# Kernel tuning notes

Measured on AMD Instinct MI355X. Metric: run time of the kernel, lower is better.

Reference implementation:

```python
import jax, jax.numpy as jnp
import numpy as np

B, T, C = 2, 2048, 1024
H, DH = 16, 64          # n_heads = d_model // 64
WIN = 256               # sliding window size
K = 32                  # n_oscillators
DFF = 4096              # d_ff_hidden
NEG = -1e9


def setup_inputs() -> dict:
    key = jax.random.key(0)
    ks = jax.random.split(key, 16)
    sC = 1.0 / np.sqrt(C)
    sF = 1.0 / np.sqrt(DFF)
    sK = 1.0 / np.sqrt(K)
    return {
        "x": jax.random.normal(ks[0], (B, T, C), jnp.float32),
        "norm1_w": jnp.ones((C,), jnp.float32),
        "qkv_w": jax.random.normal(ks[1], (3 * C, C), jnp.float32) * sC,
        "qkv_b": jnp.zeros((3 * C,), jnp.float32),
        "proj_w": jax.random.normal(ks[2], (C, C), jnp.float32) * sC,
        "proj_b": jnp.zeros((C,), jnp.float32),
        "gate_w": jax.random.normal(ks[3], (1, C), jnp.float32) * 0.01,
        "gate_b": jnp.zeros((1,), jnp.float32),
        "trn_win": jax.random.normal(ks[4], (K, C), jnp.float32) * sC,
        "trn_wout": jax.random.normal(ks[5], (C, K), jnp.float32) * sK,
        "trn_gate_w": jax.random.normal(ks[6], (K, C), jnp.float32) * sC,
        "trn_gate_b": jnp.zeros((K,), jnp.float32),
        "trn_a_logit": jax.random.normal(ks[7], (K,), jnp.float32),
        "trn_theta": jax.random.uniform(ks[8], (K,), jnp.float32, 0.0, np.pi),
        "trn_res_scale": jnp.asarray(0.1, jnp.float32),
        "norm2_w": jnp.ones((C,), jnp.float32),
        "ffn_gate_w": jax.random.normal(ks[9], (DFF, C), jnp.float32) * sC,
        "ffn_up_w": jax.random.normal(ks[10], (DFF, C), jnp.float32) * sC,
        "ffn_down_w": jax.random.normal(ks[11], (C, DFF), jnp.float32) * sF,
    }


def _rms(z, w, eps=1e-6):
    return z * jax.lax.rsqrt(jnp.mean(z * z, axis=-1, keepdims=True) + eps) * w


def reference(x, norm1_w, qkv_w, qkv_b, proj_w, proj_b, gate_w, gate_b,
              trn_win, trn_wout, trn_gate_w, trn_gate_b, trn_a_logit,
              trn_theta, trn_res_scale, norm2_w, ffn_gate_w, ffn_up_w,
              ffn_down_w):
    h = _rms(x, norm1_w)

    # ---- windowed causal attention (dense mask, as in the original) ----
    qkv = h @ qkv_w.T + qkv_b                       # [B,T,3C]
    q, k, v = jnp.split(qkv, 3, axis=-1)
    heads = lambda t: t.reshape(B, T, H, DH).transpose(0, 2, 1, 3)  # [B,H,T,DH]
    q, k, v = heads(q), heads(k), heads(v)
    row = jnp.arange(T)[:, None]
    col = jnp.arange(T)[None, :]
    mask = jnp.where((col <= row) & (col >= row - WIN + 1), 0.0, NEG).astype(x.dtype)
    scores = jnp.einsum('bhqd,bhkd->bhqk', q, k) / jnp.sqrt(jnp.asarray(DH, x.dtype))
    attn = jax.nn.softmax(scores + mask, axis=-1)
    ao = jnp.einsum('bhqk,bhkd->bhqd', attn, v).transpose(0, 2, 1, 3).reshape(B, T, C)
    ao = ao @ proj_w.T + proj_b

    # ---- temporal resonance branch: K damped rotating oscillators ----
    u = h @ trn_win.T                               # [B,T,K] drive
    a = jax.nn.sigmoid(trn_a_logit)                 # amplitude in (0,1) (amplitude_max=1)
    ct, st = jnp.cos(trn_theta), jnp.sin(trn_theta)

    def step(carry, ut):
        sr, si = carry
        nsr = a * (ct * sr - st * si) + ut
        nsi = a * (st * sr + ct * si)
        return (nsr, nsi), nsr

    init = (jnp.zeros((B, K), x.dtype), jnp.zeros((B, K), x.dtype))
    _, ys = jax.lax.scan(step, init, u.transpose(1, 0, 2))  # ys: [T,B,K]
    y = ys.transpose(1, 0, 2)                                # [B,T,K]
    tg = jax.nn.sigmoid(h @ trn_gate_w.T + trn_gate_b)
    trn_out = ((tg * y) @ trn_wout.T) * trn_res_scale        # [B,T,C]

    # ---- sigmoid gate mix + residual ----
    g = jax.nn.sigmoid(h @ gate_w.T + gate_b)       # [B,T,1]
    x = x + g * ao + (1.0 - g) * trn_out

    # ---- SwiGLU FFN ----
    h2 = _rms(x, norm2_w)
    ffn = (jax.nn.silu(h2 @ ffn_gate_w.T) * (h2 @ ffn_up_w.T)) @ ffn_down_w.T
    return x + ffn
```

## Files before the change

kernel.cpp:

```cpp
#include <hip/hip_runtime.h>


typedef unsigned short u16;
typedef unsigned short u16x8 __attribute__((ext_vector_type(8)));
typedef __bf16 bf16x8 __attribute__((ext_vector_type(8)));
typedef float f32x4 __attribute__((ext_vector_type(4)));

#define DI static __device__ __forceinline__

DI u16 f2b(float f){
  union { float f; unsigned u; } v; v.f = f;
  unsigned r = v.u + 0x7FFFu + ((v.u >> 16) & 1u);
  return (u16)(r >> 16);
}
DI float b2f(u16 b){
  union { unsigned u; float f; } v; v.u = ((unsigned)b) << 16; return v.f;
}
DI u16x8 ld8(const u16* p){ return *(const u16x8*)p; }

DI f32x4 MFMA16(u16x8 a, u16x8 b, f32x4 c){
  return __builtin_amdgcn_mfma_f32_16x16x32_bf16(
      __builtin_bit_cast(bf16x8, a), __builtin_bit_cast(bf16x8, b), c, 0, 0, 0);
}

DI void async16(const void* g, void* l){
  void* gg = const_cast<void*>(g);
  __builtin_amdgcn_global_load_lds(
      (__attribute__((address_space(1))) void*)gg,
      (__attribute__((address_space(3))) void*)l, 16, 0, 0);
}

__global__ __launch_bounds__(256) void prep_kernel(
    const float* __restrict__ qkvw, const float* __restrict__ projw,
    const float* __restrict__ fgw, const float* __restrict__ fuw,
    const float* __restrict__ fdw, const float* __restrict__ twin,
    const float* __restrict__ tgw, const float* __restrict__ twout,
    u16* __restrict__ dst,
    const float* __restrict__ x, const float* __restrict__ n1w,
    const float* __restrict__ gw, const float* __restrict__ gb,
    u16* __restrict__ h, float* __restrict__ g)
{
  const int blk = blockIdx.x, tid = threadIdx.x;
  if (blk < 16640){
    size_t i = (size_t)blk * 256 + tid;
    if (i >= 4259840u) return;
    size_t e = i * 4;
    float4 v;
    if (e < 3145728u)        v = *(const float4*)(qkvw + e);
    else if (e < 3276800u){
      size_t i2 = e - 3145728u;
      int row = (int)(i2 >> 10), c = (int)(i2 & 1023);
      if (row < 32)      v = *(const float4*)(twin + row * 1024 + c);
      else if (row < 64) v = *(const float4*)(tgw + (row - 32) * 1024 + c);
      else               v = make_float4(0.f, 0.f, 0.f, 0.f);
    }
    else if (e < 4456448u){
      unsigned i2 = (unsigned)(e - 3276800u);
      unsigned row = i2 / 1152u, kk = i2 - row * 1152u;
      if (kk < 1024u)      v = *(const float4*)(projw + (size_t)row * 1024 + kk);
      else if (kk < 1056u) v = *(const float4*)(twout + (size_t)row * 32 + (kk - 1024u));
      else                 v = make_float4(0.f, 0.f, 0.f, 0.f);
    }
    else if (e < 12845056u){
      size_t i2 = e - 4456448u;
      int row = (int)(i2 >> 10), c = (int)(i2 & 1023);
      int G = row >> 5, j = row & 31;
      const float* src = (j < 16) ? fgw : fuw;
      v = *(const float4*)(src + (size_t)(G * 16 + (j & 15)) * 1024 + c);
    }
    else                   v = *(const float4*)(fdw + (e - 12845056u));
    uint2 p;
    p.x = (unsigned)f2b(v.x) | ((unsigned)f2b(v.y) << 16);
    p.y = (unsigned)f2b(v.z) | ((unsigned)f2b(v.w) << 16);
    *(uint2*)(dst + e) = p;
    return;
  }
  const int row = blk - 16640;
  const int wave = tid >> 6, lane = tid & 63;
  __shared__ float sb[8];
  float4 xv = ((const float4*)(x + (size_t)row * 1024))[tid];
  float ss = xv.x*xv.x + xv.y*xv.y + xv.z*xv.z + xv.w*xv.w;
#pragma unroll
  for (int m = 32; m; m >>= 1) ss += __shfl_xor(ss, m);
  if (lane == 0) sb[wave] = ss;
  __syncthreads();
  float rstd = rsqrtf((sb[0]+sb[1]+sb[2]+sb[3]) * (1.f/1024.f) + 1e-6f);
  float4 wv = ((const float4*)n1w)[tid];
  float h0 = xv.x*rstd*wv.x, h1 = xv.y*rstd*wv.y;
  float h2v = xv.z*rstd*wv.z, h3 = xv.w*rstd*wv.w;
  uint2 pk;
  pk.x = (unsigned)f2b(h0) | ((unsigned)f2b(h1) << 16);
  pk.y = (unsigned)f2b(h2v) | ((unsigned)f2b(h3) << 16);
  ((uint2*)(h + (size_t)row * 1024))[tid] = pk;
  float4 gv = ((const float4*)gw)[tid];
  float gd = h0*gv.x + h1*gv.y + h2v*gv.z + h3*gv.w;
#pragma unroll
  for (int m = 32; m; m >>= 1) gd += __shfl_xor(gd, m);
  if (lane == 0) sb[4 + wave] = gd;
  __syncthreads();
  if (tid == 0) g[row] = 1.f / (1.f + __expf(-(sb[4]+sb[5]+sb[6]+sb[7] + gb[0])));
}

__global__ __launch_bounds__(256) void reduce_mix_norm(
    const u16* __restrict__ part, const float* __restrict__ x,
    const float* __restrict__ g, const float* __restrict__ pb,
    const float* __restrict__ n2w,
    float* __restrict__ out, u16* __restrict__ h2)
{
  const int row = blockIdx.x, tid = threadIdx.x;
  const int wave = tid >> 6, lane = tid & 63;
  __shared__ float sb[4];
  const size_t ro = (size_t)row * 1024;
  uint2 a0 = ((const uint2*)(part + ro))[tid];
  uint2 a1 = ((const uint2*)(part + 4194304 + ro))[tid];
  float4 bb = ((const float4*)pb)[tid];
  float4 xv = ((const float4*)(x + ro))[tid];
  float gg = g[row];
  float m0 = xv.x + b2f((u16)a0.x) + b2f((u16)a1.x) + gg*bb.x;
  float m1 = xv.y + b2f((u16)(a0.x >> 16)) + b2f((u16)(a1.x >> 16)) + gg*bb.y;
  float m2 = xv.z + b2f((u16)a0.y) + b2f((u16)a1.y) + gg*bb.z;
  float m3 = xv.w + b2f((u16)(a0.y >> 16)) + b2f((u16)(a1.y >> 16)) + gg*bb.w;
  float4 mo; mo.x = m0; mo.y = m1; mo.z = m2; mo.w = m3;
  ((float4*)(out + ro))[tid] = mo;
  float ss = m0*m0 + m1*m1 + m2*m2 + m3*m3;
#pragma unroll
  for (int m = 32; m; m >>= 1) ss += __shfl_xor(ss, m);
  if (lane == 0) sb[wave] = ss;
  __syncthreads();
  float rstd = rsqrtf((sb[0]+sb[1]+sb[2]+sb[3]) * (1.f/1024.f) + 1e-6f);
  float4 wv = ((const float4*)n2w)[tid];
  uint2 pk;
  pk.x = (unsigned)f2b(m0*rstd*wv.x) | ((unsigned)f2b(m1*rstd*wv.y) << 16);
  pk.y = (unsigned)f2b(m2*rstd*wv.z) | ((unsigned)f2b(m3*rstd*wv.w) << 16);
  ((uint2*)(h2 + ro))[tid] = pk;
}

__global__ __launch_bounds__(256) void reduce_down(
    const u16* __restrict__ part, float* __restrict__ out)
{
  size_t i = (size_t)blockIdx.x * 256 + threadIdx.x;
  uint2 a0 = ((const uint2*)part)[i];
  uint2 a1 = ((const uint2*)(part + 4194304))[i];
  uint2 a2 = ((const uint2*)(part + 8388608))[i];
  uint2 a3 = ((const uint2*)(part + 12582912))[i];
  float4 xv = ((float4*)out)[i];
  float4 o;
  o.x = xv.x + b2f((u16)a0.x) + b2f((u16)a1.x) + b2f((u16)a2.x) + b2f((u16)a3.x);
  o.y = xv.y + b2f((u16)(a0.x >> 16)) + b2f((u16)(a1.x >> 16))
             + b2f((u16)(a2.x >> 16)) + b2f((u16)(a3.x >> 16));
  o.z = xv.z + b2f((u16)a0.y) + b2f((u16)a1.y) + b2f((u16)a2.y) + b2f((u16)a3.y);
  o.w = xv.w + b2f((u16)(a0.y >> 16)) + b2f((u16)(a1.y >> 16))
             + b2f((u16)(a2.y >> 16)) + b2f((u16)(a3.y >> 16));
  ((float4*)out)[i] = o;
}

template<int MODE>
__global__ __launch_bounds__(256) void gemm_bt(
    const u16* __restrict__ A, const u16* __restrict__ B,
    float* __restrict__ outF, float* __restrict__ outF2, u16* __restrict__ outB,
    const float* __restrict__ bias, const float* __restrict__ auxF,
    int M, int N, int K)
{
  __shared__ __align__(16) u16 sA[2][128 * 32];
  __shared__ __align__(16) u16 sB[2][128 * 32];
  const int tid = threadIdx.x;
  const int wave = tid >> 6, lane = tid & 63;
  const int lr = lane & 15, lq = lane >> 4;
  const int m0 = blockIdx.x * 128, n0 = blockIdx.y * 128;
  const int wm = (wave & 1) * 64, wn = (wave >> 1) * 64;
  const int ks = K / (int)gridDim.z;
  const int kbeg = (int)blockIdx.z * ks, kend = kbeg + ks;
  f32x4 acc[4][4] = {};
  const int srow = wave * 16 + (lane >> 2);
  const int scol = (((lane & 3) ^ ((lane >> 3) & 3))) * 8;
  const u16* gA = A + (size_t)(m0 + srow) * K + scol;
  const u16* gB = B + (size_t)(n0 + srow) * K + scol;
  u16* lA0 = &sA[0][(wave * 16) * 32];
  u16* lA1 = &sA[0][(64 + wave * 16) * 32];
  u16* lB0 = &sB[0][(wave * 16) * 32];
  u16* lB1 = &sB[0][(64 + wave * 16) * 32];
  const size_t K64 = (size_t)64 * K;
  const int BUF = 128 * 32;
  const int ca = (lq ^ ((lr >> 1) & 3)) * 8;

  for (int k0 = kbeg; k0 < kend; k0 += 64){
    async16(gA + k0,            lA0);
    async16(gA + K64 + k0,      lA1);
    async16(gB + k0,            lB0);
    async16(gB + K64 + k0,      lB1);
    async16(gA + k0 + 32,       lA0 + BUF);
    async16(gA + K64 + k0 + 32, lA1 + BUF);
    async16(gB + k0 + 32,       lB0 + BUF);
    async16(gB + K64 + k0 + 32, lB1 + BUF);
    __syncthreads();
#pragma unroll
    for (int buf = 0; buf < 2; buf++){
      u16x8 af[4], bf[4];
#pragma unroll
      for (int i = 0; i < 4; i++) af[i] = ld8(&sA[buf][(wm + i*16 + lr)*32 + ca]);
#pragma unroll
      for (int i = 0; i < 4; i++) bf[i] = ld8(&sB[buf][(wn + i*16 + lr)*32 + ca]);
#pragma unroll
      for (int mi = 0; mi < 4; mi++)
#pragma unroll
        for (int ni = 0; ni < 4; ni++)
          acc[mi][ni] = MFMA16(af[mi], bf[ni], acc[mi][ni]);
    }
    __syncthreads();
  }

  if (MODE == 7){
    const int cb = ((n0 + wn) >> 1) + lr;
#pragma unroll
    for (int mi = 0; mi < 4; mi++){
      const int row = m0 + wm + mi*16 + lq*4;
#pragma unroll
      for (int p = 0; p < 2; p++){
        const int col = cb + p*16;
#pragma unroll
        for (int r = 0; r < 4; r++){
          float gv = acc[mi][2*p][r], uv = acc[mi][2*p+1][r];
          float rv = gv / (1.f + __expf(-gv)) * uv;
          outB[(size_t)(row + r) * (N >> 1) + col] = f2b(rv);
        }
      }
    }
    return;
  }

#pragma unroll
  for (int mi = 0; mi < 4; mi++){
    const int row = m0 + wm + mi*16 + lq*4;
#pragma unroll
    for (int ni = 0; ni < 4; ni++){
      const int col = n0 + wn + ni*16 + lr;
#pragma unroll
      for (int r = 0; r < 4; r++){
        const int rr = row + r;
        float v = acc[mi][ni][r];
        if (MODE == 0){
          if (n0 < 3072){
            outB[(size_t)rr * 3072 + col] = f2b(v + bias[col]);
          } else {
            int c2 = col - 3072;
            int bb = rr >> 11, tt = rr & 2047;
            if (c2 < 32) outF[((size_t)bb * 32 + c2) * 2048 + tt] = v;
            else if (c2 < 64)
              outF2[(size_t)rr * 32 + (c2 - 32)] =
                  1.f / (1.f + __expf(-(v + auxF[c2 - 32])));
          }
        } else if (MODE == 9){
          outB[(size_t)blockIdx.z * (size_t)M + (size_t)rr * N + col] = f2b(v);
        }
      }
    }
  }
}

__global__ __launch_bounds__(256) void attn_scan(
    const u16* __restrict__ qkv, const float* __restrict__ g,
    const float* __restrict__ u_t, const float* __restrict__ tg,
    const float* __restrict__ alog, const float* __restrict__ theta,
    const float* __restrict__ tscale, u16* __restrict__ Ap)
{
  __shared__ __align__(16) u16 sVt[64 * 72];
  __shared__ __align__(16) u16 sP[4][16 * 72];
  __shared__ float4 sc[256];
  const int blk = blockIdx.x, tid = threadIdx.x;

  if (blk < 1024){
    const int tile = blk & 31, hh = (blk >> 5) & 15, b = blk >> 9;
    const int t0 = tile * 64;
    const int wave = tid >> 6, lane = tid & 63;
    const int lr = lane & 15, lq = lane >> 4;
    const int qt = t0 + wave * 16;

    const u16* base = qkv + (size_t)b * 2048 * 3072 + hh * 64;
    const u16* qrow = base + (size_t)(qt + lr) * 3072 + lq * 8;
    u16x8 qf0 = ld8(qrow), qf1 = ld8(qrow + 32);
    const u16* kbase = base + 1024;
    const u16* vbase = base + 2048;

    f32x4 o0 = {0,0,0,0}, o1 = {0,0,0,0}, o2 = {0,0,0,0}, o3 = {0,0,0,0};
    float lsum[4] = {0.f, 0.f, 0.f, 0.f};
    const float c1 = 0.125f * 1.44269504088896f;

    const int kb = (t0 >= 256) ? (t0 - 256) : 0;
    const int ntl = (t0 + 64 - kb) >> 6;
    for (int it = 0; it < ntl; ++it){
      const int kt = kb + it * 64;
      __syncthreads();
      {
        const int key = tid & 63, dseg = tid >> 6;
        const u16* gv = vbase + (size_t)(kt + key) * 3072 + dseg * 16;
        u16x8 v0 = ld8(gv), v1 = ld8(gv + 8);
#pragma unroll
        for (int j = 0; j < 8; j++){
          sVt[(dseg*16 + j)     * 72 + key] = v0[j];
          sVt[(dseg*16 + 8 + j) * 72 + key] = v1[j];
        }
      }
      __syncthreads();
      const bool active = (kt < qt + 16) && (kt + 318 >= qt);
      if (!active) continue;

      f32x4 s[4] = {};
#pragma unroll
      for (int gK = 0; gK < 4; gK++){
        const u16* kr = kbase + (size_t)(kt + gK*16 + lr) * 3072 + lq * 8;
        u16x8 k0 = ld8(kr), k1 = ld8(kr + 32);
        s[gK] = MFMA16(qf0, k0, s[gK]);
        s[gK] = MFMA16(qf1, k1, s[gK]);
      }
#pragma unroll
      for (int r = 0; r < 4; r++){
        const int q = qt + lq * 4 + r;
#pragma unroll
        for (int gK = 0; gK < 4; gK++){
          const int c = kt + gK*16 + lr;
          float p = (c <= q && c + 255 >= q) ? exp2f(s[gK][r] * c1) : 0.f;
          lsum[r] += p;
          sP[wave][(lq*4 + r) * 72 + gK*16 + lr] = f2b(p);
        }
      }
      __builtin_amdgcn_s_waitcnt(0xc07f);
      u16x8 pf0 = ld8(&sP[wave][lr * 72 + lq * 8]);
      u16x8 pf1 = ld8(&sP[wave][lr * 72 + 32 + lq * 8]);
      o0 = MFMA16(pf0, ld8(&sVt[(lr)      * 72 + lq * 8]), o0);
      o0 = MFMA16(pf1, ld8(&sVt[(lr)      * 72 + 32 + lq * 8]), o0);
      o1 = MFMA16(pf0, ld8(&sVt[(16 + lr) * 72 + lq * 8]), o1);
      o1 = MFMA16(pf1, ld8(&sVt[(16 + lr) * 72 + 32 + lq * 8]), o1);
      o2 = MFMA16(pf0, ld8(&sVt[(32 + lr) * 72 + lq * 8]), o2);
      o2 = MFMA16(pf1, ld8(&sVt[(32 + lr) * 72 + 32 + lq * 8]), o2);
      o3 = MFMA16(pf0, ld8(&sVt[(48 + lr) * 72 + lq * 8]), o3);
      o3 = MFMA16(pf1, ld8(&sVt[(48 + lr) * 72 + 32 + lq * 8]), o3);
    }

#pragma unroll
    for (int r = 0; r < 4; r++){
      float l = lsum[r];
      l += __shfl_xor(l, 1); l += __shfl_xor(l, 2);
      l += __shfl_xor(l, 4); l += __shfl_xor(l, 8);
      lsum[r] = l;
    }

    const int trow = b * 2048 + qt + lq * 4;
    u16* aor = Ap + (size_t)trow * 1152 + hh * 64 + lr;
#pragma unroll
    for (int r = 0; r < 4; r++){
      float inv = g[trow + r] / lsum[r];
      u16* p = aor + (size_t)r * 1152;
      p[0]  = f2b(o0[r] * inv);
      p[16] = f2b(o1[r] * inv);
      p[32] = f2b(o2[r] * inv);
      p[48] = f2b(o3[r] * inv);
    }
    return;
  }

  if (blk < 1088){
    const int bk = blk - 1024;
    const int b = bk >> 5, k = bk & 31;
    const int j = tid;
    const float a = 1.f / (1.f + __expf(-alog[k]));
    const float th = theta[k];
    const float rs = tscale[0];
    const float wr = a * __cosf(th), wi = a * __sinf(th);
    const float* ubp = u_t + ((size_t)b * 32 + k) * 2048 + j * 8;
    float4 ua = ((const float4*)ubp)[0];
    float4 ub4 = ((const float4*)ubp)[1];
    float ur[8] = {ua.x, ua.y, ua.z, ua.w, ub4.x, ub4.y, ub4.z, ub4.w};
    float sr = 0.f, si = 0.f;
#pragma unroll
    for (int i = 0; i < 8; i++){
      float nr = wr*sr - wi*si + ur[i];
      float ni = wi*sr + wr*si;
      sr = nr; si = ni;
    }
    float w2r = wr*wr - wi*wi, w2i = 2.f*wr*wi;
    float w4r = w2r*w2r - w2i*w2i, w4i = 2.f*w2r*w2i;
    float Ar = w4r*w4r - w4i*w4i, Ai = 2.f*w4r*w4i;
    float4 cur; cur.x = Ar; cur.y = Ai; cur.z = sr; cur.w = si;
    sc[j] = cur;
    __syncthreads();
    for (int s = 1; s < 256; s <<= 1){
      float4 pv;
      const bool has = (j >= s);
      if (has) pv = sc[j - s];
      __syncthreads();
      if (has){
        float nar = cur.x*pv.x - cur.y*pv.y;
        float nai = cur.x*pv.y + cur.y*pv.x;
        float nbr = cur.x*pv.z - cur.y*pv.w + cur.z;
        float nbi = cur.x*pv.w + cur.y*pv.z + cur.w;
        cur.x = nar; cur.y = nai; cur.z = nbr; cur.w = nbi;
      }
      sc[j] = cur;
      __syncthreads();
    }
    float s_r = 0.f, s_i = 0.f;
    if (j > 0){ float4 pr = sc[j - 1]; s_r = pr.z; s_i = pr.w; }
    const int bt0 = b * 2048 + j * 8;
    const float* tgp = tg + (size_t)bt0 * 32 + k;
    u16* zp = Ap + (size_t)bt0 * 1152 + 1024 + k;
#pragma unroll
    for (int i = 0; i < 8; i++){
      float nr = wr*s_r - wi*s_i + ur[i];
      float ni = wi*s_r + wr*s_i;
      s_r = nr; s_i = ni;
      float sc2 = (1.f - g[bt0 + i]) * rs;
      zp[(size_t)i * 1152] = f2b(s_r * tgp[(size_t)i * 32] * sc2);
    }
    return;
  }

  {
    unsigned idx = (unsigned)(blk - 1088) * 256 + tid;
    unsigned row = idx / 12u, seg = idx - row * 12u;
    uint4 z4; z4.x = 0; z4.y = 0; z4.z = 0; z4.w = 0;
    *(uint4*)(Ap + (size_t)row * 1152 + 1056 + seg * 8) = z4;
  }
}

extern "C" void kernel_launch(void* const* d_in, const int* in_sizes, int n_in,
                              void* d_out, int out_size, void* d_ws, size_t ws_size,
                              hipStream_t stream)
{
  (void)in_sizes; (void)n_in; (void)out_size; (void)ws_size;
  const float* x      = (const float*)d_in[0];
  const float* n1w    = (const float*)d_in[1];
  const float* qkvw   = (const float*)d_in[2];
  const float* qkvb   = (const float*)d_in[3];
  const float* projw  = (const float*)d_in[4];
  const float* projb  = (const float*)d_in[5];
  const float* gatew  = (const float*)d_in[6];
  const float* gateb  = (const float*)d_in[7];
  const float* twin   = (const float*)d_in[8];
  const float* twout  = (const float*)d_in[9];
  const float* tgw    = (const float*)d_in[10];
  const float* tgb    = (const float*)d_in[11];
  const float* talog  = (const float*)d_in[12];
  const float* ttheta = (const float*)d_in[13];
  const float* tscale = (const float*)d_in[14];
  const float* n2w    = (const float*)d_in[15];
  const float* fgw    = (const float*)d_in[16];
  const float* fuw    = (const float*)d_in[17];
  const float* fdw    = (const float*)d_in[18];
  float* out = (float*)d_out;

  char* wsb = (char*)d_ws;
  size_t off = 0;
  auto take = [&](size_t bytes) -> void* {
    void* r = wsb + off; off += (bytes + 255) & ~(size_t)255; return r;
  };
  u16*   wall = (u16*)take(17039360ull * 2);
  u16*   h    = (u16*)take(4194304ull * 2);
  u16*   h2   = (u16*)take(4194304ull * 2);
  float* g    = (float*)take(4096ull * 4);
  float* u_t  = (float*)take(131072ull * 4);
  float* tg   = (float*)take(131072ull * 4);
  u16*   regA = (u16*)take(4096ull * 4096 * 2);
  u16*   regB = (u16*)take(4096ull * 4096 * 2);

  u16* wq  = wall;
  u16* wpx = wall + 3276800;
  u16* wgu = wall + 4456448;
  u16* wd  = wall + 12845056;
  u16* qkv    = regA;
  u16* pproj  = regA;
  u16* pdown  = regA;
  u16* Ap     = regB;
  u16* act    = regB;

  prep_kernel<<<20736, 256, 0, stream>>>(qkvw, projw, fgw, fuw, fdw, twin, tgw,
                                         twout, wall, x, n1w, gatew, gateb, h, g);
  gemm_bt<0><<<dim3(32, 25), 256, 0, stream>>>(h, wq, u_t, tg, qkv, qkvb,
                                               tgb, 0, 3200, 1024);
  attn_scan<<<1280, 256, 0, stream>>>(qkv, g, u_t, tg, talog, ttheta, tscale, Ap);
  gemm_bt<9><<<dim3(32, 8, 2), 256, 0, stream>>>(Ap, wpx, nullptr, nullptr, pproj,
                                                 nullptr, nullptr, 4194304, 1024, 1152);
  reduce_mix_norm<<<4096, 256, 0, stream>>>(pproj, x, g, projb, n2w, out, h2);
  gemm_bt<7><<<dim3(32, 64), 256, 0, stream>>>(h2, wgu, nullptr, nullptr, act, nullptr,
                                               nullptr, 0, 8192, 1024);
  gemm_bt<9><<<dim3(32, 8, 4), 256, 0, stream>>>(act, wd, nullptr, nullptr, pdown,
                                                 nullptr, nullptr, 4194304, 1024, 4096);
  reduce_down<<<4096, 256, 0, stream>>>(pdown, out);
}
```

Baseline: 420.2 us.

## Fuse split-K down-proj reduction into GEMM via semaphore; drop LDS swizzle

Removes the separate reduce_down kernel: each down-projection GEMM tile increments an atomic counter, and the last of the four split-K blocks sums the bf16 partials into the output residual. A semaphore array is zeroed by an extra block in the prep kernel. The LDS XOR swizzle on GEMM tile loads and reads is also removed, which simplifies addressing but may introduce LDS bank conflicts in all GEMMs.

```diff
diff --git a/kernel.cpp b/kernel.cpp
--- a/kernel.cpp
+++ b/kernel.cpp
@@ -38,7 +38,7 @@
     u16* __restrict__ dst,
     const float* __restrict__ x, const float* __restrict__ n1w,
     const float* __restrict__ gw, const float* __restrict__ gb,
-    u16* __restrict__ h, float* __restrict__ g)
+    u16* __restrict__ h, float* __restrict__ g, int* __restrict__ sem)
 {
   const int blk = blockIdx.x, tid = threadIdx.x;
   if (blk < 16640){
@@ -73,6 +73,10 @@
     p.x = (unsigned)f2b(v.x) | ((unsigned)f2b(v.y) << 16);
     p.y = (unsigned)f2b(v.z) | ((unsigned)f2b(v.w) << 16);
     *(uint2*)(dst + e) = p;
+    return;
+  }
+  if (blk >= 20736){
+    sem[tid] = 0;
     return;
   }
   const int row = blk - 16640;
@@ -135,30 +139,12 @@
   ((uint2*)(h2 + ro))[tid] = pk;
 }
 
-__global__ __launch_bounds__(256) void reduce_down(
-    const u16* __restrict__ part, float* __restrict__ out)
-{
-  size_t i = (size_t)blockIdx.x * 256 + threadIdx.x;
-  uint2 a0 = ((const uint2*)part)[i];
-  uint2 a1 = ((const uint2*)(part + 4194304))[i];
-  uint2 a2 = ((const uint2*)(part + 8388608))[i];
-  uint2 a3 = ((const uint2*)(part + 12582912))[i];
-  float4 xv = ((float4*)out)[i];
-  float4 o;
-  o.x = xv.x + b2f((u16)a0.x) + b2f((u16)a1.x) + b2f((u16)a2.x) + b2f((u16)a3.x);
-  o.y = xv.y + b2f((u16)(a0.x >> 16)) + b2f((u16)(a1.x >> 16))
-             + b2f((u16)(a2.x >> 16)) + b2f((u16)(a3.x >> 16));
-  o.z = xv.z + b2f((u16)a0.y) + b2f((u16)a1.y) + b2f((u16)a2.y) + b2f((u16)a3.y);
-  o.w = xv.w + b2f((u16)(a0.y >> 16)) + b2f((u16)(a1.y >> 16))
-             + b2f((u16)(a2.y >> 16)) + b2f((u16)(a3.y >> 16));
-  ((float4*)out)[i] = o;
-}
-
 template<int MODE>
 __global__ __launch_bounds__(256) void gemm_bt(
     const u16* __restrict__ A, const u16* __restrict__ B,
     float* __restrict__ outF, float* __restrict__ outF2, u16* __restrict__ outB,
     const float* __restrict__ bias, const float* __restrict__ auxF,
+    int* __restrict__ sem,
     int M, int N, int K)
 {
   __shared__ __align__(16) u16 sA[2][128 * 32];
@@ -172,7 +158,7 @@
   const int kbeg = (int)blockIdx.z * ks, kend = kbeg + ks;
   f32x4 acc[4][4] = {};
   const int srow = wave * 16 + (lane >> 2);
-  const int scol = (((lane & 3) ^ ((lane >> 3) & 3))) * 8;
+  const int scol = (lane & 3) * 8;
   const u16* gA = A + (size_t)(m0 + srow) * K + scol;
   const u16* gB = B + (size_t)(n0 + srow) * K + scol;
   u16* lA0 = &sA[0][(wave * 16) * 32];
@@ -181,7 +167,6 @@
   u16* lB1 = &sB[0][(64 + wave * 16) * 32];
   const size_t K64 = (size_t)64 * K;
   const int BUF = 128 * 32;
-  const int ca = (lq ^ ((lr >> 1) & 3)) * 8;
 
   for (int k0 = kbeg; k0 < kend; k0 += 64){
     async16(gA + k0,            lA0);
@@ -197,9 +182,9 @@
     for (int buf = 0; buf < 2; buf++){
       u16x8 af[4], bf[4];
 #pragma unroll
-      for (int i = 0; i < 4; i++) af[i] = ld8(&sA[buf][(wm + i*16 + lr)*32 + ca]);
-#pragma unroll
-      for (int i = 0; i < 4; i++) bf[i] = ld8(&sB[buf][(wn + i*16 + lr)*32 + ca]);
+      for (int i = 0; i < 4; i++) af[i] = ld8(&sA[buf][(wm + i*16 + lr)*32 + lq*8]);
+#pragma unroll
+      for (int i = 0; i < 4; i++) bf[i] = ld8(&sB[buf][(wn + i*16 + lr)*32 + lq*8]);
 #pragma unroll
       for (int mi = 0; mi < 4; mi++)
 #pragma unroll
@@ -249,9 +234,37 @@
               outF2[(size_t)rr * 32 + (c2 - 32)] =
                   1.f / (1.f + __expf(-(v + auxF[c2 - 32])));
           }
-        } else if (MODE == 9){
+        } else if (MODE == 9 || MODE == 10){
           outB[(size_t)blockIdx.z * (size_t)M + (size_t)rr * N + col] = f2b(v);
         }
+      }
+    }
+  }
+
+  if (MODE == 10){
+    __threadfence();
+    __shared__ int done;
+    if (tid == 0)
+      done = atomicAdd(&sem[blockIdx.x * 8 + blockIdx.y], 1);
+    __syncthreads();
+    if (done == 3){
+      __threadfence();
+#pragma unroll
+      for (int i = 0; i < 16; i++){
+        const int idx = tid * 16 + i;
+        const int rloc = idx >> 5, c4 = idx & 31;
+        const size_t base = (size_t)(m0 + rloc) * 1024 + (n0 + c4 * 4);
+        float s0 = 0.f, s1 = 0.f, s2 = 0.f, s3 = 0.f;
+#pragma unroll
+        for (int z = 0; z < 4; z++){
+          uint2 a = *(const uint2*)(outB + (size_t)z * 4194304 + base);
+          s0 += b2f((u16)a.x); s1 += b2f((u16)(a.x >> 16));
+          s2 += b2f((u16)a.y); s3 += b2f((u16)(a.y >> 16));
+        }
+        float4 xv = *(const float4*)(outF + base);
+        float4 o;
+        o.x = xv.x + s0; o.y = xv.y + s1; o.z = xv.z + s2; o.w = xv.w + s3;
+        *(float4*)(outF + base) = o;
       }
     }
   }
@@ -459,6 +472,7 @@
   float* g    = (float*)take(4096ull * 4);
   float* u_t  = (float*)take(131072ull * 4);
   float* tg   = (float*)take(131072ull * 4);
+  int*   sem  = (int*)take(256ull * 4);
   u16*   regA = (u16*)take(4096ull * 4096 * 2);
   u16*   regB = (u16*)take(4096ull * 4096 * 2);
 
@@ -472,17 +486,18 @@
   u16* Ap     = regB;
   u16* act    = regB;
 
-  prep_kernel<<<20736, 256, 0, stream>>>(qkvw, projw, fgw, fuw, fdw, twin, tgw,
-                                         twout, wall, x, n1w, gatew, gateb, h, g);
+  prep_kernel<<<20737, 256, 0, stream>>>(qkvw, projw, fgw, fuw, fdw, twin, tgw,
+                                         twout, wall, x, n1w, gatew, gateb, h, g, sem);
   gemm_bt<0><<<dim3(32, 25), 256, 0, stream>>>(h, wq, u_t, tg, qkv, qkvb,
-                                               tgb, 0, 3200, 1024);
+                                               tgb, nullptr, 0, 3200, 1024);
   attn_scan<<<1280, 256, 0, stream>>>(qkv, g, u_t, tg, talog, ttheta, tscale, Ap);
   gemm_bt<9><<<dim3(32, 8, 2), 256, 0, stream>>>(Ap, wpx, nullptr, nullptr, pproj,
-                                                 nullptr, nullptr, 4194304, 1024, 1152);
+                                                 nullptr, nullptr, nullptr,
+                                                 4194304, 1024, 1152);
   reduce_mix_norm<<<4096, 256, 0, stream>>>(pproj, x, g, projb, n2w, out, h2);
   gemm_bt<7><<<dim3(32, 64), 256, 0, stream>>>(h2, wgu, nullptr, nullptr, act, nullptr,
-                                               nullptr, 0, 8192, 1024);
-  gemm_bt<9><<<dim3(32, 8, 4), 256, 0, stream>>>(act, wd, nullptr, nullptr, pdown,
-                                                 nullptr, nullptr, 4194304, 1024, 4096);
-  reduce_down<<<4096, 256, 0, stream>>>(pdown, out);
-}
+                                               nullptr, nullptr, 0, 8192, 1024);
+  gemm_bt<10><<<dim3(32, 8, 4), 256, 0, stream>>>(act, wd, out, nullptr, pdown,
+                                                  nullptr, nullptr, sem,
+                                                  4194304, 1024, 4096);
+}
```

Result: slower. 579.6 us (+37.9%).
